# Performance work log

Hardware: AMD Instinct MI355X
Metric: run time of the kernel (lower is better)

Reference implementation:

```python
import jax, jax.numpy as jnp
import numpy as np

B, S, E, H = 4, 2048, 1024, 16
D = E // H  # head_size = 64


def setup_inputs() -> dict:
    key = jax.random.key(0)
    ks = jax.random.split(key, 5)
    x = jax.random.normal(ks[0], (B, S, E), dtype=jnp.float32)
    # nn.Linear default init ~ U(-1/sqrt(fan_in), 1/sqrt(fan_in))
    bound = 1.0 / np.sqrt(E)
    W_qkv = jax.random.uniform(ks[1], (E, 3 * E), dtype=jnp.float32, minval=-bound, maxval=bound)
    b_qkv = jax.random.uniform(ks[2], (3 * E,), dtype=jnp.float32, minval=-bound, maxval=bound)
    W_out = jax.random.uniform(ks[3], (E, E), dtype=jnp.float32, minval=-bound, maxval=bound)
    b_out = jax.random.uniform(ks[4], (E,), dtype=jnp.float32, minval=-bound, maxval=bound)
    return {"x": x, "W_qkv": W_qkv, "b_qkv": b_qkv, "W_out": W_out, "b_out": b_out, "mask": 1}


def reference(x, W_qkv, b_qkv, W_out, b_out, mask):
    qkv = x @ W_qkv + b_qkv                              # [B,S,3E]
    qkv = qkv.reshape(B, S, H, 3 * D).transpose(0, 2, 1, 3)  # [B,H,S,3D]
    q, k, v = jnp.split(qkv, 3, axis=-1)                  # each [B,H,S,D]
    scale = 1.0 / np.sqrt(E)  # NOTE: original divides by sqrt(n_embd), not sqrt(head_size)
    y = jnp.einsum('bhqd,bhkd->bhqk', q, k) * scale       # [B,H,S,S]
    if mask:
        causal = jnp.tril(jnp.ones((S, S), dtype=bool))
        y = jnp.where(causal, y, -1e9)
    y = jax.nn.softmax(y, axis=-1)
    vals = jnp.einsum('bhqk,bhkd->bhqd', y, v)            # [B,H,S,D]
    vals = vals.transpose(0, 2, 1, 3).reshape(B, S, E)
    return vals @ W_out + b_out
```

## Files before the change

### kernel.cpp

```cpp
#include <hip/hip_runtime.h>
#include <hip/hip_bf16.h>
#include <cstdint>
#include <cstddef>

typedef __bf16 bf16;
typedef __bf16 bf16x8 __attribute__((ext_vector_type(8)));
typedef float f32x4 __attribute__((ext_vector_type(4)));
typedef unsigned int u32x4 __attribute__((ext_vector_type(4)));
typedef unsigned int u32x2 __attribute__((ext_vector_type(2)));

#define DEVINL __device__ __forceinline__

namespace {
constexpr int Bb = 4, Ss = 2048, Ee = 1024, Hh = 16;
constexpr int Mm = Bb * Ss;
constexpr int N_QKV = 3 * Ee;
constexpr float SCQ = 0.03125f * 1.44269504f;
}

DEVINL void gl_lds16(const bf16* g, bf16* l) {
  __builtin_amdgcn_global_load_lds((const __attribute__((address_space(1))) void*)g,
                                   (__attribute__((address_space(3))) void*)l, 16, 0, 0);
}

DEVINL unsigned int pkbf(float a, float b) {
  bf16 x = (bf16)a, y = (bf16)b;
  return (unsigned int)__builtin_bit_cast(unsigned short, x) |
         ((unsigned int)__builtin_bit_cast(unsigned short, y) << 16);
}


__global__ __launch_bounds__(256) void k_prep(const float* __restrict__ x, bf16* __restrict__ x_bf,
                                              const float* __restrict__ Wqkv, bf16* __restrict__ WqkvT,
                                              const float* __restrict__ Wout, bf16* __restrict__ WoutT) {
  __shared__ float tile[32][33];
  const int gb = blockIdx.x;
  if (gb < 4096) {
    const int i = (gb * 256 + threadIdx.x) * 8;
    float4 a = *(const float4*)(x + i);
    float4 c = *(const float4*)(x + i + 4);
    bf16x8 v = {(bf16)a.x, (bf16)a.y, (bf16)a.z, (bf16)a.w,
                (bf16)c.x, (bf16)c.y, (bf16)c.z, (bf16)c.w};
    *(bf16x8*)(x_bf + i) = v;
    return;
  }
  const float* in;
  bf16* outp;
  int R, C, bx, by;
  if (gb < 4096 + 3072) {
    const int g = gb - 4096;
    in = Wqkv; outp = WqkvT; R = Ee; C = N_QKV;
    bx = g % 96; by = g / 96;
  } else {
    const int g = gb - 4096 - 3072;
    in = Wout; outp = WoutT; R = Ee; C = Ee;
    bx = g % 32; by = g / 32;
  }
  const int c0 = bx * 32, r0 = by * 32;
  const int tx = threadIdx.x & 31, ty = threadIdx.x >> 5;
  for (int i = 0; i < 32; i += 8)
    tile[ty + i][tx] = in[(size_t)(r0 + ty + i) * C + (c0 + tx)];
  __syncthreads();
  for (int i = 0; i < 32; i += 8)
    outp[(size_t)(c0 + ty + i) * R + (r0 + tx)] = (bf16)tile[tx][ty + i];
}


template <int NF>
DEVINL void gemm_core256(const bf16* __restrict__ A, const bf16* __restrict__ Bt,
                         int m0, int n0, bf16* As, bf16* Bs, f32x4 (&acc)[8][NF]) {
  constexpr int K = 1024;
  constexpr int TILEA = 16384;
  constexpr int TILEB = NF * 4096;
  const int tid = threadIdx.x;
  const int w = tid >> 6, lane = tid & 63;
  const int wm = w >> 2, wn = w & 3;
  const int fr = lane & 15, kg = lane >> 4;
  const int gc = (tid & 7) ^ ((tid >> 3) & 7);
  const int srow = tid >> 3;
  const bf16* Ag = A + (size_t)(m0 + srow) * K + gc * 8;
  const bf16* Bg = Bt + (size_t)(n0 + srow) * K + gc * 8;
  bf16* AdW = As + w * 512;
  bf16* BdW = Bs + w * 512;

#define STAGE_TILE(kt, buf)                                                       \
  {                                                                               \
    for (int i = 0; i < 4; ++i)                                                   \
      gl_lds16(Ag + (kt) + (size_t)(i * 64) * K, AdW + (buf) * TILEA + i * 4096); \
    for (int i = 0; i < NF; ++i)                                                  \
      gl_lds16(Bg + (kt) + (size_t)(i * 64) * K, BdW + (buf) * TILEB + i * 4096); \
  }

  STAGE_TILE(0, 0)
  STAGE_TILE(64, 1)
  constexpr int nt = K / 64;
  for (int t = 0; t < nt; ++t) {
    const int cur = t & 1;
    if constexpr (NF == 3) {
      asm volatile("s_waitcnt vmcnt(7)" ::: "memory");
    } else {
      asm volatile("s_waitcnt vmcnt(6)" ::: "memory");
    }
    __builtin_amdgcn_sched_barrier(0);
    __builtin_amdgcn_s_barrier();
    __builtin_amdgcn_sched_barrier(0);
    bf16x8 af[2][8], bfx[2][NF];
    const bf16* Ab = As + cur * TILEA;
    const bf16* Bb = Bs + cur * TILEB;
    for (int kk = 0; kk < 2; ++kk) {
      const int sw = ((kk * 4 + kg) ^ (fr & 7)) * 8;
      for (int mi = 0; mi < 8; ++mi)
        af[kk][mi] = *(const bf16x8*)(Ab + (wm * 128 + mi * 16 + fr) * 64 + sw);
      for (int ni = 0; ni < NF; ++ni)
        bfx[kk][ni] = *(const bf16x8*)(Bb + (wn * (NF * 16) + ni * 16 + fr) * 64 + sw);
    }
    asm volatile("s_waitcnt lgkmcnt(0)" ::: "memory");
    __builtin_amdgcn_sched_barrier(0);
    __builtin_amdgcn_s_barrier();
    __builtin_amdgcn_sched_barrier(0);
    if (t + 2 < nt) STAGE_TILE((t + 2) * 64, cur)
    __builtin_amdgcn_s_setprio(1);
    for (int kk = 0; kk < 2; ++kk)
      for (int mi = 0; mi < 8; ++mi)
        for (int ni = 0; ni < NF; ++ni)
          acc[mi][ni] =
              __builtin_amdgcn_mfma_f32_16x16x32_bf16(af[kk][mi], bfx[kk][ni], acc[mi][ni], 0, 0, 0);
    __builtin_amdgcn_s_setprio(0);
  }
#undef STAGE_TILE
}

__global__ __launch_bounds__(512, 2) void k_qkv_gemm(const bf16* __restrict__ A,
                                                     const bf16* __restrict__ Bt,
                                                     const float* __restrict__ bias,
                                                     bf16* __restrict__ qbuf,
                                                     bf16* __restrict__ kbuf,
                                                     bf16* __restrict__ vtb) {
  __shared__ bf16 As[2 * 16384];
  __shared__ bf16 Bs[2 * 3 * 4096];
  const int m0 = blockIdx.y * 256, n0 = blockIdx.x * 192;
  f32x4 acc[8][3] = {};
  gemm_core256<3>(A, Bt, m0, n0, As, Bs, acc);

  const int tid = threadIdx.x, w = tid >> 6, lane = tid & 63;
  const int wm = w >> 2, wn = w & 3;
  const int fr = lane & 15, kg = lane >> 4;
  const int row_b = m0 >> 11;
  for (int ni = 0; ni < 3; ++ni) {
    const int col0 = n0 + wn * 48 + ni * 16;
    const int h = col0 / 192;
    const int w192 = col0 - h * 192;
    const int cls = w192 >> 6;
    const float bv = bias[col0 + fr];
    if (cls == 2) {
      const int d = w192 - 128 + fr;
      bf16* dstb = vtb + (((size_t)row_b * Hh + h) * 64 + d) * Ss;
      for (int mi = 0; mi < 8; ++mi) {
        const int s0 = (m0 & 2047) + wm * 128 + mi * 16 + kg * 4;
        u32x2 pk2 = {pkbf(acc[mi][ni][0] + bv, acc[mi][ni][1] + bv),
                     pkbf(acc[mi][ni][2] + bv, acc[mi][ni][3] + bv)};
        *(u32x2*)(dstb + s0) = pk2;
      }
    } else {
      bf16* buf = (cls == 0) ? qbuf : kbuf;
      const float sc = (cls == 0) ? SCQ : 1.f;
      const int d = (w192 & 63) + fr;
      bf16* dstb = buf + ((size_t)row_b * Hh + h) * Ss * 64 + d;
      for (int mi = 0; mi < 8; ++mi) {
        const int s0 = (m0 & 2047) + wm * 128 + mi * 16 + kg * 4;
        for (int r = 0; r < 4; ++r)
          dstb[(size_t)(s0 + r) * 64] = (bf16)((acc[mi][ni][r] + bv) * sc);
      }
    }
  }
}

__global__ __launch_bounds__(512, 2) void k_out_gemm(const bf16* __restrict__ A,
                                                     const bf16* __restrict__ Bt,
                                                     const float* __restrict__ bias,
                                                     float* __restrict__ out) {
  __shared__ bf16 As[2 * 16384];
  __shared__ bf16 Bs[2 * 2 * 4096];
  const int m0 = blockIdx.y * 256, n0 = blockIdx.x * 128;
  f32x4 acc[8][2] = {};
  gemm_core256<2>(A, Bt, m0, n0, As, Bs, acc);

  const int tid = threadIdx.x, w = tid >> 6, lane = tid & 63;
  const int wm = w >> 2, wn = w & 3;
  const int fr = lane & 15, kg = lane >> 4;
  for (int ni = 0; ni < 2; ++ni) {
    const int col = n0 + wn * 32 + ni * 16 + fr;
    const float bv = bias[col];
    for (int mi = 0; mi < 8; ++mi) {
      const int mb = m0 + wm * 128 + mi * 16 + kg * 4;
      for (int r = 0; r < 4; ++r)
        out[(size_t)(mb + r) * Ee + col] = acc[mi][ni][r] + bv;
    }
  }
}


__global__ __launch_bounds__(256, 3) void k_attn(const bf16* __restrict__ qbuf,
                                                 const bf16* __restrict__ kbuf,
                                                 const bf16* __restrict__ vtb,
                                                 bf16* __restrict__ vals) {
  const int g = blockIdx.x;
  const int qt = 15 - (g >> 6);
  const int bh = g & 63;
  const int b = bh >> 4, h = bh & 15;
  const int q0 = qt * 128;
  const int tid = threadIdx.x, w = tid >> 6, lane = tid & 63;
  const int fr = lane & 15, kg = lane >> 4;
  const int rl = lane >> 3, cl = (lane & 7) ^ (lane >> 3);

  __shared__ bf16 KsB[2][4096];
  __shared__ bf16 VtB[2][4096];

  const bf16* qb = qbuf + (size_t)bh * Ss * 64;
  const bf16* kb = kbuf + (size_t)bh * Ss * 64 + (size_t)rl * 64 + cl * 8;
  const bf16* vb = vtb + (size_t)bh * 64 * Ss + (size_t)rl * Ss + cl * 8;

  const int gA = (kg & 1) * 32 + fr;
  const int gB = gA + 16;
  const bool hiSel = (kg >> 1) != 0;

  bf16x8 aq[2][2];
  for (int sub = 0; sub < 2; ++sub) {
    const bf16* qr = qb + (size_t)(q0 + w * 32 + sub * 16 + fr) * 64 + kg * 8;
    aq[sub][0] = *(const bf16x8*)(qr);
    aq[sub][1] = *(const bf16x8*)(qr + 32);
  }

  float m_run[2] = {-1e30f, -1e30f}, l_run[2] = {0.f, 0.f};
  f32x4 o_acc[2][4] = {};

  const int nt = 2 * qt + 2;

  for (int t = 0; t < 2; ++t) {
    const int i = w * 2 + t;
    gl_lds16(kb + (size_t)(i * 8) * 64, KsB[0] + i * 512);
    gl_lds16(vb + (size_t)(i * 8) * Ss, VtB[0] + i * 512);
  }

  int cur = 0;
  for (int it = 0; it < nt; ++it) {
    const int kv0 = it * 64;
    __syncthreads();
    if (it + 1 < nt) {
      const int kvn = kv0 + 64;
      for (int t = 0; t < 2; ++t) {
        const int i = w * 2 + t;
        gl_lds16(kb + (size_t)(kvn + i * 8) * 64, KsB[cur ^ 1] + i * 512);
        gl_lds16(vb + (size_t)(i * 8) * Ss + kvn, VtB[cur ^ 1] + i * 512);
      }
    }
    const bool active = (kv0 <= q0 + w * 32 + 31);
    if (active) {
      f32x4 sacc[2][4] = {};
      for (int kk = 0; kk < 2; ++kk) {
        bf16x8 bk[4];
        for (int ni = 0; ni < 4; ++ni) {
          const int rb = ni * 16 + fr;
          bk[ni] = *(const bf16x8*)(KsB[cur] + rb * 64 + (((kk * 4 + kg) ^ (rb & 7)) * 8));
        }
        __builtin_amdgcn_s_setprio(1);
        for (int sub = 0; sub < 2; ++sub)
          for (int ni = 0; ni < 4; ++ni)
            sacc[sub][ni] =
                __builtin_amdgcn_mfma_f32_16x16x32_bf16(bk[ni], aq[sub][kk], sacc[sub][ni], 0, 0, 0);
        __builtin_amdgcn_s_setprio(0);
      }
      bf16x8 bp[2][2];
      for (int sub = 0; sub < 2; ++sub) {
        const int qs = q0 + w * 32 + sub * 16;
        float p[4][4];
        float mnew = -1e30f;
        if (kv0 + 63 > qs) {
          const int q = qs + fr;
          for (int ni = 0; ni < 4; ++ni)
            for (int r = 0; r < 4; ++r) {
              const int k = kv0 + ni * 16 + kg * 4 + r;
              float s = sacc[sub][ni][r];
              if (k > q) s = -1e30f;
              p[ni][r] = s;
              mnew = fmaxf(mnew, s);
            }
        } else {
          for (int ni = 0; ni < 4; ++ni)
            for (int r = 0; r < 4; ++r) {
              float s = sacc[sub][ni][r];
              p[ni][r] = s;
              mnew = fmaxf(mnew, s);
            }
        }
        mnew = fmaxf(mnew, __shfl_xor(mnew, 16, 64));
        mnew = fmaxf(mnew, __shfl_xor(mnew, 32, 64));
        float mn;
        if (__all(mnew - m_run[sub] <= 8.f)) {
          mn = m_run[sub];
        } else {
          mn = fmaxf(m_run[sub], mnew);
          const float fs = exp2f(m_run[sub] - mn);
          m_run[sub] = mn;
          l_run[sub] *= fs;
          for (int ni = 0; ni < 4; ++ni)
            for (int r = 0; r < 4; ++r)
              o_acc[sub][ni][r] *= fs;
        }
        float rs = 0.f;
        for (int ni = 0; ni < 4; ++ni)
          for (int r = 0; r < 4; ++r) {
            const float e = exp2f(p[ni][r] - mn);
            p[ni][r] = e;
            rs += e;
          }
        rs += __shfl_xor(rs, 16, 64);
        rs += __shfl_xor(rs, 32, 64);
        l_run[sub] += rs;
        unsigned int Wlo[4], Whi[4];
        for (int ni = 0; ni < 4; ++ni) {
          Wlo[ni] = pkbf(p[ni][0], p[ni][1]);
          Whi[ni] = pkbf(p[ni][2], p[ni][3]);
        }
        for (int kk = 0; kk < 2; ++kk) {
          const int i0 = 2 * kk, i1 = 2 * kk + 1;
          unsigned int a0 = (unsigned int)__shfl((int)Wlo[i0], gA, 64);
          unsigned int a1 = (unsigned int)__shfl((int)Wlo[i1], gA, 64);
          unsigned int b0 = (unsigned int)__shfl((int)Whi[i0], gA, 64);
          unsigned int b1 = (unsigned int)__shfl((int)Whi[i1], gA, 64);
          unsigned int c0 = (unsigned int)__shfl((int)Wlo[i0], gB, 64);
          unsigned int c1 = (unsigned int)__shfl((int)Wlo[i1], gB, 64);
          unsigned int d0 = (unsigned int)__shfl((int)Whi[i0], gB, 64);
          unsigned int d1 = (unsigned int)__shfl((int)Whi[i1], gB, 64);
          u32x4 wv = {hiSel ? a1 : a0, hiSel ? b1 : b0, hiSel ? c1 : c0, hiSel ? d1 : d0};
          bp[sub][kk] = __builtin_bit_cast(bf16x8, wv);
        }
      }
      for (int kk = 0; kk < 2; ++kk) {
        bf16x8 bv[4];
        for (int ni = 0; ni < 4; ++ni) {
          const int rb = ni * 16 + fr;
          bv[ni] = *(const bf16x8*)(VtB[cur] + rb * 64 + (((kk * 4 + kg) ^ (rb & 7)) * 8));
        }
        __builtin_amdgcn_s_setprio(1);
        for (int sub = 0; sub < 2; ++sub)
          for (int ni = 0; ni < 4; ++ni)
            o_acc[sub][ni] =
                __builtin_amdgcn_mfma_f32_16x16x32_bf16(bv[ni], bp[sub][kk], o_acc[sub][ni], 0, 0, 0);
        __builtin_amdgcn_s_setprio(0);
      }
    }
    cur ^= 1;
  }

  for (int sub = 0; sub < 2; ++sub) {
    const float inv = 1.f / l_run[sub];
    const int q = q0 + w * 32 + sub * 16 + fr;
    bf16* dst = vals + ((size_t)b * Ss + q) * Ee + h * 64 + kg * 4;
    for (int ni = 0; ni < 4; ++ni) {
      u32x2 pk2 = {pkbf(o_acc[sub][ni][0] * inv, o_acc[sub][ni][1] * inv),
                   pkbf(o_acc[sub][ni][2] * inv, o_acc[sub][ni][3] * inv)};
      *(u32x2*)(dst + ni * 16) = pk2;
    }
  }
}


extern "C" void kernel_launch(void* const* d_in, const int* in_sizes, int n_in,
                              void* d_out, int out_size, void* d_ws, size_t ws_size,
                              hipStream_t stream) {
  const float* x    = (const float*)d_in[0];
  const float* Wqkv = (const float*)d_in[1];
  const float* bqkv = (const float*)d_in[2];
  const float* Wout = (const float*)d_in[3];
  const float* bout = (const float*)d_in[4];
  float* out = (float*)d_out;

  char* ws = (char*)d_ws;
  const size_t MiB = 1048576, KiB = 1024;
  bf16* x_bf  = (bf16*)(ws);
  bf16* valsb = (bf16*)(ws);
  bf16* WqkvT = (bf16*)(ws + 16 * MiB);
  bf16* WoutT = (bf16*)(ws + 22 * MiB);
  bf16* qbuf  = (bf16*)(ws + 24 * MiB);
  bf16* kbuf  = (bf16*)(ws + 40 * MiB + 192 * KiB);
  bf16* vtb   = (bf16*)(ws + 56 * MiB + 384 * KiB);

  k_prep<<<dim3(4096 + 3072 + 1024), dim3(256), 0, stream>>>(x, x_bf, Wqkv, WqkvT, Wout, WoutT);
  k_qkv_gemm<<<dim3(N_QKV / 192, Mm / 256), dim3(512), 0, stream>>>(x_bf, WqkvT, bqkv, qbuf, kbuf, vtb);
  k_attn<<<dim3(Ss / 128 * Hh * Bb), dim3(256), 0, stream>>>(qbuf, kbuf, vtb, valsb);
  k_out_gemm<<<dim3(Ee / 128, Mm / 256), dim3(512), 0, stream>>>(valsb, WoutT, bout, out);
}
```

Before: 187.2 us.

## Split GEMM main loop into two phases with finer-grained async staging

Restructures the shared GEMM core so each K-step runs in two halves. Each half loads half of the A fragments from LDS and issues half of the next tile's global-to-LDS copies, which shortens prefetch distance from two tiles to one. Splitting the A fragments also lowers register pressure. In exchange it adds barriers per iteration and exposes more global load latency.

```diff
diff --git a/kernel.cpp b/kernel.cpp
--- a/kernel.cpp
+++ b/kernel.cpp
@@ -67,7 +67,7 @@
 
 
 template <int NF>
-DEVINL void gemm_core256(const bf16* __restrict__ A, const bf16* __restrict__ Bt,
+DEVINL void gemm_core2ph(const bf16* __restrict__ A, const bf16* __restrict__ Bt,
                          int m0, int n0, bf16* As, bf16* Bs, f32x4 (&acc)[8][NF]) {
   constexpr int K = 1024;
   constexpr int TILEA = 16384;
@@ -83,34 +83,34 @@
   bf16* AdW = As + w * 512;
   bf16* BdW = Bs + w * 512;
 
-#define STAGE_TILE(kt, buf)                                                       \
-  {                                                                               \
-    for (int i = 0; i < 4; ++i)                                                   \
-      gl_lds16(Ag + (kt) + (size_t)(i * 64) * K, AdW + (buf) * TILEA + i * 4096); \
-    for (int i = 0; i < NF; ++i)                                                  \
-      gl_lds16(Bg + (kt) + (size_t)(i * 64) * K, BdW + (buf) * TILEB + i * 4096); \
-  }
-
-  STAGE_TILE(0, 0)
-  STAGE_TILE(64, 1)
+#define STA_U(kt, buf, i) gl_lds16(Ag + (kt) + (size_t)((i) * 64) * K, AdW + (buf) * TILEA + (i) * 4096);
+#define STB_U(kt, buf, i) gl_lds16(Bg + (kt) + (size_t)((i) * 64) * K, BdW + (buf) * TILEB + (i) * 4096);
+#define STAGE_PA(kt, buf)                      \
+  {                                            \
+    STA_U(kt, buf, 0)                          \
+    STA_U(kt, buf, 2)                          \
+    for (int i = 0; i < NF; ++i) STB_U(kt, buf, i) \
+  }
+#define STAGE_PB(kt, buf) { STA_U(kt, buf, 1) STA_U(kt, buf, 3) }
+
+  STAGE_PA(0, 0)
+  STAGE_PB(0, 0)
   constexpr int nt = K / 64;
   for (int t = 0; t < nt; ++t) {
-    const int cur = t & 1;
-    if constexpr (NF == 3) {
-      asm volatile("s_waitcnt vmcnt(7)" ::: "memory");
-    } else {
-      asm volatile("s_waitcnt vmcnt(6)" ::: "memory");
-    }
-    __builtin_amdgcn_sched_barrier(0);
-    __builtin_amdgcn_s_barrier();
-    __builtin_amdgcn_sched_barrier(0);
-    bf16x8 af[2][8], bfx[2][NF];
+    const int cur = t & 1, nxt = cur ^ 1;
+    const int kt2 = (t + 1) * 64;
     const bf16* Ab = As + cur * TILEA;
     const bf16* Bb = Bs + cur * TILEB;
+    asm volatile("s_waitcnt vmcnt(2)" ::: "memory");
+    __builtin_amdgcn_sched_barrier(0);
+    __builtin_amdgcn_s_barrier();
+    __builtin_amdgcn_sched_barrier(0);
+    if (t + 1 < nt) STAGE_PA(kt2, nxt)
+    bf16x8 afl[2][4], bfx[2][NF];
     for (int kk = 0; kk < 2; ++kk) {
       const int sw = ((kk * 4 + kg) ^ (fr & 7)) * 8;
-      for (int mi = 0; mi < 8; ++mi)
-        af[kk][mi] = *(const bf16x8*)(Ab + (wm * 128 + mi * 16 + fr) * 64 + sw);
+      for (int mi = 0; mi < 4; ++mi)
+        afl[kk][mi] = *(const bf16x8*)(Ab + (wm * 128 + mi * 16 + fr) * 64 + sw);
       for (int ni = 0; ni < NF; ++ni)
         bfx[kk][ni] = *(const bf16x8*)(Bb + (wn * (NF * 16) + ni * 16 + fr) * 64 + sw);
     }
@@ -118,16 +118,48 @@
     __builtin_amdgcn_sched_barrier(0);
     __builtin_amdgcn_s_barrier();
     __builtin_amdgcn_sched_barrier(0);
-    if (t + 2 < nt) STAGE_TILE((t + 2) * 64, cur)
     __builtin_amdgcn_s_setprio(1);
     for (int kk = 0; kk < 2; ++kk)
-      for (int mi = 0; mi < 8; ++mi)
+      for (int mi = 0; mi < 4; ++mi)
         for (int ni = 0; ni < NF; ++ni)
           acc[mi][ni] =
-              __builtin_amdgcn_mfma_f32_16x16x32_bf16(af[kk][mi], bfx[kk][ni], acc[mi][ni], 0, 0, 0);
+              __builtin_amdgcn_mfma_f32_16x16x32_bf16(afl[kk][mi], bfx[kk][ni], acc[mi][ni], 0, 0, 0);
     __builtin_amdgcn_s_setprio(0);
-  }
-#undef STAGE_TILE
+    if (t + 1 < nt) {
+      if constexpr (NF == 3) {
+        asm volatile("s_waitcnt vmcnt(5)" ::: "memory");
+      } else {
+        asm volatile("s_waitcnt vmcnt(4)" ::: "memory");
+      }
+    } else {
+      asm volatile("s_waitcnt vmcnt(0)" ::: "memory");
+    }
+    __builtin_amdgcn_sched_barrier(0);
+    __builtin_amdgcn_s_barrier();
+    __builtin_amdgcn_sched_barrier(0);
+    if (t + 1 < nt) STAGE_PB(kt2, nxt)
+    bf16x8 afh[2][4];
+    for (int kk = 0; kk < 2; ++kk) {
+      const int sw = ((kk * 4 + kg) ^ (fr & 7)) * 8;
+      for (int mi = 0; mi < 4; ++mi)
+        afh[kk][mi] = *(const bf16x8*)(Ab + (wm * 128 + (mi + 4) * 16 + fr) * 64 + sw);
+    }
+    asm volatile("s_waitcnt lgkmcnt(0)" ::: "memory");
+    __builtin_amdgcn_sched_barrier(0);
+    __builtin_amdgcn_s_barrier();
+    __builtin_amdgcn_sched_barrier(0);
+    __builtin_amdgcn_s_setprio(1);
+    for (int kk = 0; kk < 2; ++kk)
+      for (int mi = 0; mi < 4; ++mi)
+        for (int ni = 0; ni < NF; ++ni)
+          acc[mi + 4][ni] =
+              __builtin_amdgcn_mfma_f32_16x16x32_bf16(afh[kk][mi], bfx[kk][ni], acc[mi + 4][ni], 0, 0, 0);
+    __builtin_amdgcn_s_setprio(0);
+  }
+#undef STAGE_PA
+#undef STAGE_PB
+#undef STA_U
+#undef STB_U
 }
 
 __global__ __launch_bounds__(512, 2) void k_qkv_gemm(const bf16* __restrict__ A,
@@ -140,7 +172,7 @@
   __shared__ bf16 Bs[2 * 3 * 4096];
   const int m0 = blockIdx.y * 256, n0 = blockIdx.x * 192;
   f32x4 acc[8][3] = {};
-  gemm_core256<3>(A, Bt, m0, n0, As, Bs, acc);
+  gemm_core2ph<3>(A, Bt, m0, n0, As, Bs, acc);
 
   const int tid = threadIdx.x, w = tid >> 6, lane = tid & 63;
   const int wm = w >> 2, wn = w & 3;
@@ -183,7 +215,7 @@
   __shared__ bf16 Bs[2 * 2 * 4096];
   const int m0 = blockIdx.y * 256, n0 = blockIdx.x * 128;
   f32x4 acc[8][2] = {};
-  gemm_core256<2>(A, Bt, m0, n0, As, Bs, acc);
+  gemm_core2ph<2>(A, Bt, m0, n0, As, Bs, acc);
 
   const int tid = threadIdx.x, w = tid >> 6, lane = tid & 63;
   const int wm = w >> 2, wn = w & 3;
```

New measurement: 212.3 us. +13.4%, slower.
